# Performance work log

Hardware: AMD Instinct MI355X
Metric: run time of the kernel (lower is better)

Reference implementation:

```python
import jax, jax.numpy as jnp
import numpy as np

D_MODEL = 1024
NUM_HEADS = 16
D_HEAD = 64
D_MLP = 4096
SEQ = 2048
BATCH = 4
NEG_BIG = 1e10


def setup_inputs() -> dict:
    key = jax.random.key(0)
    ks = jax.random.split(key, 10)
    s = 1.0 / np.sqrt(D_MODEL)
    return {
        "x": jax.random.normal(ks[0], (BATCH, SEQ, D_MODEL), dtype=jnp.float32),
        "W_K": jax.random.normal(ks[1], (NUM_HEADS, D_HEAD, D_MODEL), dtype=jnp.float32) * s,
        "W_Q": jax.random.normal(ks[2], (NUM_HEADS, D_HEAD, D_MODEL), dtype=jnp.float32) * s,
        "W_V": jax.random.normal(ks[3], (NUM_HEADS, D_HEAD, D_MODEL), dtype=jnp.float32) * s,
        "W_O": jax.random.normal(ks[4], (D_MODEL, D_HEAD * NUM_HEADS), dtype=jnp.float32) * s,
        "W_in": jax.random.normal(ks[5], (D_MLP, D_MODEL), dtype=jnp.float32) * s,
        "b_in": jnp.zeros((D_MLP,), dtype=jnp.float32),
        "W_out": jax.random.normal(ks[6], (D_MODEL, D_MLP), dtype=jnp.float32) * s,
        "b_out": jnp.zeros((D_MODEL,), dtype=jnp.float32),
    }


def _block(x, W_K, W_Q, W_V, W_O, W_in, b_in, W_out, b_out):
    seq = x.shape[1]
    # Attention
    k = jnp.einsum("ihd,bpd->biph", W_K, x)
    q = jnp.einsum("ihd,bpd->biph", W_Q, x)
    v = jnp.einsum("ihd,bpd->biph", W_V, x)
    scores = jnp.einsum("biph,biqh->biqp", k, q)  # [b, i, q(query), p(key)]
    mask = jnp.tril(jnp.ones((seq, seq), dtype=x.dtype))  # causal: key p <= query q
    scores = scores * mask - NEG_BIG * (1.0 - mask)
    attn = jax.nn.softmax(scores / np.sqrt(D_HEAD), axis=-1)
    z = jnp.einsum("biph,biqp->biqh", v, attn)  # [b, heads, q, d_head]
    z_flat = jnp.transpose(z, (0, 2, 1, 3)).reshape(z.shape[0], seq, -1)  # b q (i h)
    attn_out = jnp.einsum("df,bqf->bqd", W_O, z_flat)
    x = x + attn_out
    # MLP
    h = jnp.einsum("md,bpd->bpm", W_in, x) + b_in
    h = jax.nn.gelu(h, approximate=False)
    mlp_out = jnp.einsum("dm,bpm->bpd", W_out, h) + b_out
    return x + mlp_out


def reference(x, W_K, W_Q, W_V, W_O, W_in, b_in, W_out, b_out):
    return _block(x, W_K, W_Q, W_V, W_O, W_in, b_in, W_out, b_out)
```

## Files before the change

kernel.cpp:

```cpp
#include <hip/hip_runtime.h>
#include <hip/hip_bf16.h>

typedef __bf16 bf16;
typedef __bf16 bf16x8 __attribute__((ext_vector_type(8)));
typedef __bf16 bf16x4 __attribute__((ext_vector_type(4)));
typedef float  f32x4  __attribute__((ext_vector_type(4)));

#define MFMA(a,b,c) __builtin_amdgcn_mfma_f32_16x16x32_bf16(a,b,c,0,0,0)
#define EXP2F(x) __builtin_amdgcn_exp2f(x)

__device__ __forceinline__ void gload16(const void* g, void* l) {
  __builtin_amdgcn_global_load_lds((__attribute__((address_space(1))) void*)(g),
                                   (__attribute__((address_space(3))) void*)(l), 16, 0, 0);
}

struct CastSegs {
  const float* src[7];
  bf16* dst[7];
  int cum[8];
};

__global__ void cast_multi(CastSegs s) {
  int i = blockIdx.x * 256 + threadIdx.x;
  if (i >= s.cum[7]) return;
  int k = 0;
  #pragma unroll
  for (int j = 1; j < 7; ++j) if (i >= s.cum[j]) k = j;
  int off = i - s.cum[k];
  const float4* p = (const float4*)s.src[k];
  float4 a = p[2*off], b = p[2*off+1];
  bf16x8 v;
  v[0]=(bf16)a.x; v[1]=(bf16)a.y; v[2]=(bf16)a.z; v[3]=(bf16)a.w;
  v[4]=(bf16)b.x; v[5]=(bf16)b.y; v[6]=(bf16)b.z; v[7]=(bf16)b.w;
  *(bf16x8*)(s.dst[k] + (size_t)8*off) = v;
}

__device__ __forceinline__ float gelu_t(float s) {
  float u = s * (0.7978845608f + 0.0356774081f * s * s);
  return s / (1.0f + EXP2F(-2.885390082f * u));
}

#define LGKM0_FENCE() { asm volatile("s_waitcnt lgkmcnt(0)" ::: "memory"); \
                        __builtin_amdgcn_sched_barrier(0); }


#define LDA_PH(MI2) { _Pragma("unroll") for (int i = 0; i < 4; i++) { \
    af[i][0] = *(const bf16x8*)(lds + ab + ((((MI2)<<2)+i) << 11) + rdswz); \
    af[i][1] = *(const bf16x8*)(lds + ab + ((((MI2)<<2)+i) << 11) + 1024 + rdswz); } }

#define LDB_PH(NI2) { _Pragma("unroll") for (int n = 0; n < 2; n++) { \
    bfr[((NI2)<<1)+n][0] = *(const bf16x8*)(lds + bb + (((((NI2)<<1)+n)) << 11) + rdswz); \
    bfr[((NI2)<<1)+n][1] = *(const bf16x8*)(lds + bb + (((((NI2)<<1)+n)) << 11) + 1024 + rdswz); } }

#define MM_PH(MI2, NI2) { __builtin_amdgcn_s_setprio(1); \
    _Pragma("unroll") for (int i = 0; i < 4; i++) \
      _Pragma("unroll") for (int n = 0; n < 2; n++) { \
        acc[((MI2)<<2)+i][((NI2)<<1)+n] = MFMA(af[i][0], bfr[((NI2)<<1)+n][0], acc[((MI2)<<2)+i][((NI2)<<1)+n]); \
        acc[((MI2)<<2)+i][((NI2)<<1)+n] = MFMA(af[i][1], bfr[((NI2)<<1)+n][1], acc[((MI2)<<2)+i][((NI2)<<1)+n]); } \
    __builtin_amdgcn_s_setprio(0); }

#define GTILE(CUR, S1, S2, VM) { \
    const int ab = ((CUR) << 16) + (wm << 14); \
    const int bb = ((CUR) << 16) + 32768 + (wn << 13); \
    LDA_PH(0); LDB_PH(0); \
    if (S1) STG(sA, (CUR)^1, 0, 1, t + 1); \
    asm volatile("s_waitcnt lgkmcnt(8)" ::: "memory"); \
    __builtin_amdgcn_s_barrier(); LGKM0_FENCE(); \
    MM_PH(0, 0); \
    LDB_PH(1); \
    if (S2) STG(sB, (CUR), 1, 0, t + 2); \
    __builtin_amdgcn_s_barrier(); LGKM0_FENCE(); \
    MM_PH(0, 1); \
    LDA_PH(1); \
    if (S2) STG(sB, (CUR), 1, 1, t + 2); \
    __builtin_amdgcn_s_barrier(); LGKM0_FENCE(); \
    MM_PH(1, 0); \
    if (S2) STG(sA, (CUR), 0, 0, t + 2); \
    MM_PH(1, 1); \
    asm volatile("s_waitcnt vmcnt(" #VM ")" ::: "memory"); \
    __builtin_amdgcn_s_barrier(); \
    __builtin_amdgcn_sched_barrier(0); }

template<int EPI>
__global__ __launch_bounds__(512, 2) void gemm256(
    const bf16* __restrict__ A, const bf16* __restrict__ B,
    float* __restrict__ outf, bf16* __restrict__ outb,
    const bf16* __restrict__ addb, const float* __restrict__ bias,
    bf16* __restrict__ vtb,
    int M, int N, int K, int gx)
{
  __shared__ __attribute__((aligned(128))) char lds[131072];
  const int tid = threadIdx.x;
  const int w = tid >> 6, l = tid & 63, lg = l >> 4, li = l & 15;
  const int wm = w >> 2, wn = w & 3;

  const int nwg = gridDim.x, orig = blockIdx.x;
  const int q = nwg >> 3, r = nwg & 7;
  const int xcd = orig & 7, pos = orig >> 3;
  const int wg = (xcd < r ? xcd*(q+1) : r*(q+1) + (xcd-r)*q) + pos;
  const int m0 = (wg / gx) << 8, n0 = (wg % gx) << 8;

  const int NT = K >> 6;

  const int srow = ((tid >> 7) << 4) + ((tid >> 2) & 15);
  const int scol = (((tid >> 6) & 1) << 5) + (((tid & 3) << 3) ^ (((tid >> 5) & 1) << 4));
  const bf16* sA = A + (size_t)(m0 + srow) * K + scol;
  const bf16* sB = B + (size_t)(n0 + srow) * K + scol;
  char* const myl = lds + (w << 10);

  auto STG = [&](const bf16* s0, int buf, int isB, int h, int tt) {
    const bf16* g = s0 + ((size_t)(h << 7)) * K + ((size_t)tt << 6);
    char* lb = myl + (buf << 16) + (isB << 15) + (h << 14);
    gload16(g, lb);
    gload16(g + ((size_t)K << 6), lb + 8192);
  };

  const int rdswz = (li << 6) + ((lg << 4) ^ ((li & 8) << 2));

  f32x4 acc[8][4] = {};
  bf16x8 af[4][2], bfr[4][2];

  STG(sB, 0, 1, 0, 0); STG(sB, 0, 1, 1, 0); STG(sA, 0, 0, 0, 0); STG(sA, 0, 0, 1, 0);
  asm volatile("s_waitcnt vmcnt(4)" ::: "memory");
  STG(sB, 1, 1, 0, 1); STG(sB, 1, 1, 1, 1); STG(sA, 1, 0, 0, 1);
  asm volatile("s_waitcnt vmcnt(6)" ::: "memory");
  __builtin_amdgcn_s_barrier();
  __builtin_amdgcn_sched_barrier(0);

  int t = 0;
  for (int tt = 0; tt + 3 < NT; tt += 2) {
    t = tt;     GTILE(0, 1, 1, 6);
    t = tt + 1; GTILE(1, 1, 1, 6);
  }
  t = NT - 2; GTILE(0, 1, 0, 0);
  t = NT - 1; GTILE(1, 0, 0, 0);

  if (EPI == 0 && n0 >= 2048) {
    #pragma unroll
    for (int mi = 0; mi < 8; mi++) {
      const int row = m0 + (wm << 7) + (mi << 4) + (lg << 2);
      const int p = row & 2047;
      const size_t bhb = (size_t)((row >> 11) << 4);
      #pragma unroll
      for (int ni = 0; ni < 4; ni++) {
        const int col = n0 + (wn << 6) + (ni << 4) + li;
        const int hh = (col >> 6) & 15, dd = col & 63;
        bf16x4 pk;
        pk[0] = (bf16)acc[mi][ni][0]; pk[1] = (bf16)acc[mi][ni][1];
        pk[2] = (bf16)acc[mi][ni][2]; pk[3] = (bf16)acc[mi][ni][3];
        *(bf16x4*)(vtb + ((bhb + hh) * 64 + dd) * 2048 + p) = pk;
      }
    }
    return;
  }

  #pragma unroll
  for (int mi = 0; mi < 8; mi++) {
    const int row = m0 + (wm << 7) + (mi << 4) + (lg << 2);
    #pragma unroll
    for (int ni = 0; ni < 4; ni++) {
      const int col = n0 + (wn << 6) + (ni << 4) + li;
      #pragma unroll
      for (int r2 = 0; r2 < 4; r2++) {
        const size_t idx = (size_t)(row + r2) * N + col;
        float v = acc[mi][ni][r2];
        if (EPI == 0) {
          outb[idx] = (bf16)v;
        } else if (EPI == 1) {
          outb[idx] = (bf16)(v + (float)addb[idx]);
        } else if (EPI == 2) {
          outb[idx] = (bf16)gelu_t(v + bias[col]);
        } else {
          outf[idx] = v + bias[col] + (float)addb[idx];
        }
      }
    }
  }
}

#define N_LDA2(BMI) { _Pragma("unroll") for (int i = 0; i < 2; i++) { \
    af[i][0] = *(const bf16x8*)(lds + abase + (((BMI)+i) << 11) + rdswz); \
    af[i][1] = *(const bf16x8*)(lds + abase + (((BMI)+i) << 11) + 1024 + rdswz); } }

#define N_LDB2(BNI) { _Pragma("unroll") for (int n = 0; n < 2; n++) { \
    bfr[(BNI)+n][0] = *(const bf16x8*)(lds + bbase + (((BNI)+n) << 11) + rdswz); \
    bfr[(BNI)+n][1] = *(const bf16x8*)(lds + bbase + (((BNI)+n) << 11) + 1024 + rdswz); } }

#define N_MMQ(MB, NB) { __builtin_amdgcn_s_setprio(1); \
    _Pragma("unroll") for (int i = 0; i < 2; i++) \
      _Pragma("unroll") for (int n = 0; n < 2; n++) { \
        acc[((MB)<<1)+i][((NB)<<1)+n] = MFMA(af[i][0], bfr[((NB)<<1)+n][0], acc[((MB)<<1)+i][((NB)<<1)+n]); \
        acc[((MB)<<1)+i][((NB)<<1)+n] = MFMA(af[i][1], bfr[((NB)<<1)+n][1], acc[((MB)<<1)+i][((NB)<<1)+n]); } \
    __builtin_amdgcn_s_setprio(0); }

#define NTILE(CUR, S1, S2, VM) { \
    const int abase = (CUR) * 49152 + ((wm >> 1) << 14) + ((wm & 1) << 13); \
    const int bbase = (CUR) * 49152 + 32768 + (wn << 13); \
    N_LDA2(0); N_LDB2(0); \
    if (S1) STA((CUR)^1, 1, t + 1); \
    __builtin_amdgcn_s_barrier(); LGKM0_FENCE(); \
    N_MMQ(0, 0); \
    N_LDB2(2); \
    if (S2) STB((CUR), 0, t + 2); \
    __builtin_amdgcn_s_barrier(); LGKM0_FENCE(); \
    N_MMQ(0, 1); \
    N_LDA2(2); \
    if (S2) STB((CUR), 1, t + 2); \
    __builtin_amdgcn_s_barrier(); LGKM0_FENCE(); \
    N_MMQ(1, 0); \
    if (S2) STA((CUR), 0, t + 2); \
    N_MMQ(1, 1); \
    asm volatile("s_waitcnt vmcnt(" #VM ")" ::: "memory"); \
    __builtin_amdgcn_s_barrier(); \
    __builtin_amdgcn_sched_barrier(0); }

template<int EPI>
__global__ __launch_bounds__(512, 2) void gemm128n(
    const bf16* __restrict__ A, const bf16* __restrict__ B,
    float* __restrict__ outf, bf16* __restrict__ outb,
    const bf16* __restrict__ addb, const float* __restrict__ bias,
    bf16* __restrict__ vtb,
    int M, int N, int K, int gx)
{
  __shared__ __attribute__((aligned(128))) char lds[98304];
  const int tid = threadIdx.x;
  const int w = tid >> 6, l = tid & 63, lg = l >> 4, li = l & 15;
  const int wm = w >> 1, wn = w & 1;

  const int nwg = gridDim.x, orig = blockIdx.x;
  const int q = nwg >> 3, r = nwg & 7;
  const int xcd = orig & 7, pos = orig >> 3;
  const int wg = (xcd < r ? xcd*(q+1) : r*(q+1) + (xcd-r)*q) + pos;
  const int m0 = (wg / gx) << 8, n0 = (wg % gx) << 7;

  const int NT = K >> 6;

  const int srow = ((tid >> 7) << 4) + ((tid >> 2) & 15);
  const int scol = (((tid >> 6) & 1) << 5) + (((tid & 3) << 3) ^ (((tid >> 5) & 1) << 4));
  const bf16* sA = A + (size_t)(m0 + srow) * K + scol;
  const bf16* sB = B + (size_t)(n0 + srow) * K + scol;
  char* const myl = lds + (w << 10);

  auto STA = [&](int buf, int h, int tt) {
    const bf16* g = sA + ((size_t)(h << 7)) * K + ((size_t)tt << 6);
    char* lb = myl + buf * 49152 + (h << 14);
    gload16(g, lb);
    gload16(g + ((size_t)K << 6), lb + 8192);
  };
  auto STB = [&](int buf, int h, int tt) {
    const bf16* g = sB + ((size_t)(h << 6)) * K + ((size_t)tt << 6);
    gload16(g, myl + buf * 49152 + 32768 + (h << 13));
  };

  const int rdswz = (li << 6) + ((lg << 4) ^ ((li & 8) << 2));

  f32x4 acc[4][4] = {};
  bf16x8 af[2][2], bfr[4][2];

  STB(0, 0, 0); STB(0, 1, 0); STA(0, 0, 0); STA(0, 1, 0);
  STB(1, 0, 1); STB(1, 1, 1); STA(1, 0, 1);
  asm volatile("s_waitcnt vmcnt(4)" ::: "memory");
  __builtin_amdgcn_s_barrier();
  __builtin_amdgcn_sched_barrier(0);

  int t = 0;
  for (int tt = 0; tt + 3 < NT; tt += 2) {
    t = tt;     NTILE(0, 1, 1, 4);
    t = tt + 1; NTILE(1, 1, 1, 4);
  }
  t = NT - 2; NTILE(0, 1, 0, 0);
  t = NT - 1; NTILE(1, 0, 0, 0);

  if (EPI == 0 && n0 >= 2048) {
    #pragma unroll
    for (int mi = 0; mi < 4; mi++) {
      const int row = m0 + (wm << 6) + (mi << 4) + (lg << 2);
      const int p = row & 2047;
      const size_t bhb = (size_t)((row >> 11) << 4);
      #pragma unroll
      for (int ni = 0; ni < 4; ni++) {
        const int col = n0 + (wn << 6) + (ni << 4) + li;
        const int hh = (col >> 6) & 15, dd = col & 63;
        bf16x4 pk;
        pk[0] = (bf16)acc[mi][ni][0]; pk[1] = (bf16)acc[mi][ni][1];
        pk[2] = (bf16)acc[mi][ni][2]; pk[3] = (bf16)acc[mi][ni][3];
        *(bf16x4*)(vtb + ((bhb + hh) * 64 + dd) * 2048 + p) = pk;
      }
    }
    return;
  }

  #pragma unroll
  for (int mi = 0; mi < 4; mi++) {
    const int row = m0 + (wm << 6) + (mi << 4) + (lg << 2);
    #pragma unroll
    for (int ni = 0; ni < 4; ni++) {
      const int col = n0 + (wn << 6) + (ni << 4) + li;
      #pragma unroll
      for (int r2 = 0; r2 < 4; r2++) {
        const size_t idx = (size_t)(row + r2) * N + col;
        float v = acc[mi][ni][r2];
        if (EPI == 0) {
          outb[idx] = (bf16)v;
        } else if (EPI == 1) {
          outb[idx] = (bf16)(v + (float)addb[idx]);
        } else if (EPI == 2) {
          outb[idx] = (bf16)gelu_t(v + bias[col]);
        } else {
          outf[idx] = v + bias[col] + (float)addb[idx];
        }
      }
    }
  }
}

__global__ __launch_bounds__(256) void attn_kernel(const bf16* __restrict__ qkv,
                                                   const bf16* __restrict__ vt,
                                                   bf16* __restrict__ z)
{
  __shared__ bf16 Ksh[2][64*64];
  __shared__ bf16 Vsh[2][64*64];
  __shared__ bf16 Pl[4*16*64];

  const int tid = threadIdx.x;
  const int w = tid >> 6, l = tid & 63, lg = l >> 4, li = l & 15;
  const int orig = blockIdx.x;
  const int xcd = orig & 7, sub = orig >> 3;
  const int bh = (xcd << 3) + (sub >> 4);
  const int pr = sub & 15;
  const int h = bh & 15, b = bh >> 4;
  const size_t tb = (size_t)b * 2048;

  const int srow = tid >> 3, sc = tid & 7;
  const bf16* Kg = qkv + (tb + srow) * 3072 + 1024 + (h << 6) + ((sc ^ (srow & 7)) << 3);
  const bf16* Vg = vt + ((size_t)bh * 64 + srow) * 2048 + ((sc ^ (srow & 7)) << 3);

  char* pw = (char*)Pl + (w << 11) + li * 128;
  const int psw = (li & 3) << 5;

  for (int hf = 0; hf < 2; ++hf) {
    const int qt = hf ? pr : (31 - pr);
    const int qw = (qt << 6) + (w << 4);

    const bf16* Qp = qkv + (tb + qw + li) * 3072 + (h << 6);
    bf16x8 qa0 = *(const bf16x8*)(Qp + (lg << 3));
    bf16x8 qa1 = *(const bf16x8*)(Qp + 32 + (lg << 3));
    #pragma unroll
    for (int e = 0; e < 8; e++) {
      qa0[e] = (bf16)((float)qa0[e] * 0.1803368801f);
      qa1[e] = (bf16)((float)qa1[e] * 0.1803368801f);
    }

    f32x4 zacc[4] = {};
    float lS = 0.f;
    const int nkt = qt + 1;

    gload16(Kg,                   (bf16*)Ksh[0] + (w << 9));
    gload16(Kg + (size_t)32*3072, (bf16*)Ksh[0] + 2048 + (w << 9));
    gload16(Vg,                   (bf16*)Vsh[0] + (w << 9));
    gload16(Vg + (size_t)32*2048, (bf16*)Vsh[0] + 2048 + (w << 9));
    __syncthreads();

    for (int kt = 0; kt < nkt; ++kt) {
      const int cur = kt & 1;
      const int pb = kt << 6;

      if (kt + 1 < nkt) {
        const int nb = cur ^ 1;
        const size_t ko = (size_t)(pb + 64) * 3072;
        gload16(Kg + ko,                   (bf16*)Ksh[nb] + (w << 9));
        gload16(Kg + ko + (size_t)32*3072, (bf16*)Ksh[nb] + 2048 + (w << 9));
        gload16(Vg + pb + 64,                   (bf16*)Vsh[nb] + (w << 9));
        gload16(Vg + pb + 64 + (size_t)32*2048, (bf16*)Vsh[nb] + 2048 + (w << 9));
      }

      f32x4 s[4];
      __builtin_amdgcn_s_setprio(1);
      #pragma unroll
      for (int sub2 = 0; sub2 < 4; ++sub2) {
        const char* kr = (const char*)Ksh[cur] + ((sub2 << 4) + li) * 128;
        const int c0 = (lg ^ (li & 7)) << 4;
        bf16x8 kb0 = *(const bf16x8*)(kr + c0);
        bf16x8 kb1 = *(const bf16x8*)(kr + (c0 ^ 64));
        f32x4 a2 = {};
        a2 = MFMA(kb0, qa0, a2);
        a2 = MFMA(kb1, qa1, a2);
        s[sub2] = a2;
      }
      __builtin_amdgcn_s_setprio(0);

      if (pb + 63 > qw) {
        #pragma unroll
        for (int sub2 = 0; sub2 < 4; ++sub2)
          #pragma unroll
          for (int r = 0; r < 4; ++r)
            if (pb + (sub2 << 4) + (lg << 2) + r > qw + li) s[sub2][r] = -1e30f;
      }

      f32x4 p[4];
      #pragma unroll
      for (int sub2 = 0; sub2 < 4; ++sub2)
        #pragma unroll
        for (int r = 0; r < 4; ++r)
          p[sub2][r] = EXP2F(s[sub2][r]);
      f32x4 t4 = p[0] + p[1] + p[2] + p[3];
      lS += (t4[0] + t4[1]) + (t4[2] + t4[3]);

      #pragma unroll
      for (int sub2 = 0; sub2 < 4; ++sub2) {
        bf16x4 pk;
        pk[0] = (bf16)p[sub2][0]; pk[1] = (bf16)p[sub2][1];
        pk[2] = (bf16)p[sub2][2]; pk[3] = (bf16)p[sub2][3];
        *(bf16x4*)(pw + (((sub2 << 5) + (lg << 3)) ^ psw)) = pk;
      }

      __builtin_amdgcn_s_setprio(1);
      #pragma unroll
      for (int kc = 0; kc < 2; ++kc) {
        bf16x8 pa = *(const bf16x8*)(pw + (((kc << 6) + (lg << 4)) ^ psw));
        #pragma unroll
        for (int d = 0; d < 4; ++d) {
          const char* vr = (const char*)Vsh[cur] + ((d << 4) + li) * 128;
          bf16x8 vb = *(const bf16x8*)(vr + ((((kc << 2) + lg) ^ (li & 7)) << 4));
          zacc[d] = MFMA(pa, vb, zacc[d]);
        }
      }
      __builtin_amdgcn_s_setprio(0);

      __syncthreads();
    }

    lS += __shfl_xor(lS, 16);
    lS += __shfl_xor(lS, 32);

    float rls[4];
    #pragma unroll
    for (int r = 0; r < 4; ++r) rls[r] = 1.0f / __shfl(lS, (lg << 2) + r);
    bf16* zp = z + (tb + qw) * 1024 + (h << 6);
    #pragma unroll
    for (int d = 0; d < 4; ++d)
      #pragma unroll
      for (int r = 0; r < 4; ++r)
        zp[(size_t)((lg << 2) + r) * 1024 + (d << 4) + li] = (bf16)(zacc[d][r] * rls[r]);
  }
}

extern "C" void kernel_launch(void* const* d_in, const int* in_sizes, int n_in,
                              void* d_out, int out_size, void* d_ws, size_t ws_size,
                              hipStream_t stream)
{
  const float* x     = (const float*)d_in[0];
  const float* W_K   = (const float*)d_in[1];
  const float* W_Q   = (const float*)d_in[2];
  const float* W_V   = (const float*)d_in[3];
  const float* W_O   = (const float*)d_in[4];
  const float* W_in  = (const float*)d_in[5];
  const float* b_in  = (const float*)d_in[6];
  const float* W_out = (const float*)d_in[7];
  const float* b_out = (const float*)d_in[8];
  float* out = (float*)d_out;

  char* ws = (char*)d_ws;
  bf16*  xb   = (bf16*)ws;  ws += (size_t)8192*1024*2;
  bf16*  wqkv = (bf16*)ws;  ws += (size_t)3072*1024*2;
  bf16*  wo   = (bf16*)ws;  ws += (size_t)1024*1024*2;
  bf16*  win  = (bf16*)ws;  ws += (size_t)4096*1024*2;
  bf16*  wout = (bf16*)ws;  ws += (size_t)1024*4096*2;
  bf16*  qkv  = (bf16*)ws;  ws += (size_t)8192*3072*2;
  bf16*  zb   = (bf16*)ws;  ws += (size_t)8192*1024*2;
  bf16*  x1b  = (bf16*)ws;  ws += (size_t)8192*1024*2;
  bf16*  hb   = (bf16*)ws;
  bf16*  vtb  = hb;

  CastSegs cs;
  const float* srcs[7] = { x, W_Q, W_K, W_V, W_O, W_in, W_out };
  bf16* dsts[7] = { xb, wqkv, wqkv + 1024*1024, wqkv + 2048*1024, wo, win, wout };
  int n8s[7] = { 1048576, 131072, 131072, 131072, 131072, 524288, 524288 };
  int cum = 0;
  for (int i = 0; i < 7; ++i) { cs.src[i] = srcs[i]; cs.dst[i] = dsts[i]; cs.cum[i] = cum; cum += n8s[i]; }
  cs.cum[7] = cum;
  cast_multi<<<dim3((cum + 255) / 256), dim3(256), 0, stream>>>(cs);

  gemm128n<0><<<dim3(768), 512, 0, stream>>>(xb, wqkv, nullptr, qkv, nullptr, nullptr, vtb, 8192, 3072, 1024, 24);
  attn_kernel<<<dim3(1024), 256, 0, stream>>>(qkv, vtb, zb);
  gemm128n<1><<<dim3(256), 512, 0, stream>>>(zb, wo, nullptr, x1b, xb, nullptr, nullptr, 8192, 1024, 1024, 8);
  gemm256<2><<<dim3(512), 512, 0, stream>>>(x1b, win, nullptr, hb, nullptr, b_in, nullptr, 8192, 4096, 1024, 16);
  gemm128n<3><<<dim3(256), 512, 0, stream>>>(hb, wout, out, nullptr, x1b, b_out, nullptr, 8192, 1024, 4096, 8);
}
```

Measured before the change: 290.6 us.

## Double attention query tile per block to reuse K/V LDS tiles

Each attention block now handles 128 query rows instead of 64, with each wave processing two 16-row groups. Every K/V tile loaded into LDS therefore feeds twice as many MFMAs, which halves global K/V traffic and the number of barriers per query. The grid shrinks from 1024 to 512 blocks, and the P staging buffer in LDS doubles. In exchange, per-wave register pressure rises and there are fewer blocks to balance the causal workload across CUs.

New measurement: 325.9 us. 12.1% more time.

```diff
diff --git a/kernel.cpp b/kernel.cpp
--- a/kernel.cpp
+++ b/kernel.cpp
@@ -320,14 +320,14 @@
 {
   __shared__ bf16 Ksh[2][64*64];
   __shared__ bf16 Vsh[2][64*64];
-  __shared__ bf16 Pl[4*16*64];
+  __shared__ bf16 Pl[4*32*64];
 
   const int tid = threadIdx.x;
   const int w = tid >> 6, l = tid & 63, lg = l >> 4, li = l & 15;
   const int orig = blockIdx.x;
   const int xcd = orig & 7, sub = orig >> 3;
-  const int bh = (xcd << 3) + (sub >> 4);
-  const int pr = sub & 15;
+  const int bh = (xcd << 3) + (sub >> 3);
+  const int pr = sub & 7;
   const int h = bh & 15, b = bh >> 4;
   const size_t tb = (size_t)b * 2048;
 
@@ -335,25 +335,29 @@
   const bf16* Kg = qkv + (tb + srow) * 3072 + 1024 + (h << 6) + ((sc ^ (srow & 7)) << 3);
   const bf16* Vg = vt + ((size_t)bh * 64 + srow) * 2048 + ((sc ^ (srow & 7)) << 3);
 
-  char* pw = (char*)Pl + (w << 11) + li * 128;
+  char* pw = (char*)Pl + (w << 12) + li * 128;
   const int psw = (li & 3) << 5;
 
   for (int hf = 0; hf < 2; ++hf) {
-    const int qt = hf ? pr : (31 - pr);
-    const int qw = (qt << 6) + (w << 4);
-
-    const bf16* Qp = qkv + (tb + qw + li) * 3072 + (h << 6);
-    bf16x8 qa0 = *(const bf16x8*)(Qp + (lg << 3));
-    bf16x8 qa1 = *(const bf16x8*)(Qp + 32 + (lg << 3));
+    const int qt = hf ? pr : (15 - pr);
+    const int qw = (qt << 7) + (w << 5);
+
+    bf16x8 qa0[2], qa1[2];
     #pragma unroll
-    for (int e = 0; e < 8; e++) {
-      qa0[e] = (bf16)((float)qa0[e] * 0.1803368801f);
-      qa1[e] = (bf16)((float)qa1[e] * 0.1803368801f);
-    }
-
-    f32x4 zacc[4] = {};
-    float lS = 0.f;
-    const int nkt = qt + 1;
+    for (int g = 0; g < 2; ++g) {
+      const bf16* Qp = qkv + (tb + qw + (g << 4) + li) * 3072 + (h << 6);
+      qa0[g] = *(const bf16x8*)(Qp + (lg << 3));
+      qa1[g] = *(const bf16x8*)(Qp + 32 + (lg << 3));
+      #pragma unroll
+      for (int e = 0; e < 8; e++) {
+        qa0[g][e] = (bf16)((float)qa0[g][e] * 0.1803368801f);
+        qa1[g][e] = (bf16)((float)qa1[g][e] * 0.1803368801f);
+      }
+    }
+
+    f32x4 zacc[2][4] = {};
+    float lS0 = 0.f, lS1 = 0.f;
+    const int nkt = (qt + 1) << 1;
 
     gload16(Kg,                   (bf16*)Ksh[0] + (w << 9));
     gload16(Kg + (size_t)32*3072, (bf16*)Ksh[0] + 2048 + (w << 9));
@@ -374,7 +378,7 @@
         gload16(Vg + pb + 64 + (size_t)32*2048, (bf16*)Vsh[nb] + 2048 + (w << 9));
       }
 
-      f32x4 s[4];
+      f32x4 s[2][4];
       __builtin_amdgcn_s_setprio(1);
       #pragma unroll
       for (int sub2 = 0; sub2 < 4; ++sub2) {
@@ -382,47 +386,58 @@
         const int c0 = (lg ^ (li & 7)) << 4;
         bf16x8 kb0 = *(const bf16x8*)(kr + c0);
         bf16x8 kb1 = *(const bf16x8*)(kr + (c0 ^ 64));
-        f32x4 a2 = {};
-        a2 = MFMA(kb0, qa0, a2);
-        a2 = MFMA(kb1, qa1, a2);
-        s[sub2] = a2;
+        #pragma unroll
+        for (int g = 0; g < 2; ++g) {
+          f32x4 a2 = {};
+          a2 = MFMA(kb0, qa0[g], a2);
+          a2 = MFMA(kb1, qa1[g], a2);
+          s[g][sub2] = a2;
+        }
       }
       __builtin_amdgcn_s_setprio(0);
 
       if (pb + 63 > qw) {
+        #pragma unroll
+        for (int g = 0; g < 2; ++g)
+          #pragma unroll
+          for (int sub2 = 0; sub2 < 4; ++sub2)
+            #pragma unroll
+            for (int r = 0; r < 4; ++r)
+              if (pb + (sub2 << 4) + (lg << 2) + r > qw + (g << 4) + li)
+                s[g][sub2][r] = -1e30f;
+      }
+
+      #pragma unroll
+      for (int g = 0; g < 2; ++g) {
+        f32x4 p[4];
         #pragma unroll
         for (int sub2 = 0; sub2 < 4; ++sub2)
           #pragma unroll
           for (int r = 0; r < 4; ++r)
-            if (pb + (sub2 << 4) + (lg << 2) + r > qw + li) s[sub2][r] = -1e30f;
-      }
-
-      f32x4 p[4];
-      #pragma unroll
-      for (int sub2 = 0; sub2 < 4; ++sub2)
+            p[sub2][r] = EXP2F(s[g][sub2][r]);
+        f32x4 t4 = p[0] + p[1] + p[2] + p[3];
+        float sm = (t4[0] + t4[1]) + (t4[2] + t4[3]);
+        if (g == 0) lS0 += sm; else lS1 += sm;
         #pragma unroll
-        for (int r = 0; r < 4; ++r)
-          p[sub2][r] = EXP2F(s[sub2][r]);
-      f32x4 t4 = p[0] + p[1] + p[2] + p[3];
-      lS += (t4[0] + t4[1]) + (t4[2] + t4[3]);
-
-      #pragma unroll
-      for (int sub2 = 0; sub2 < 4; ++sub2) {
-        bf16x4 pk;
-        pk[0] = (bf16)p[sub2][0]; pk[1] = (bf16)p[sub2][1];
-        pk[2] = (bf16)p[sub2][2]; pk[3] = (bf16)p[sub2][3];
-        *(bf16x4*)(pw + (((sub2 << 5) + (lg << 3)) ^ psw)) = pk;
+        for (int sub2 = 0; sub2 < 4; ++sub2) {
+          bf16x4 pk;
+          pk[0] = (bf16)p[sub2][0]; pk[1] = (bf16)p[sub2][1];
+          pk[2] = (bf16)p[sub2][2]; pk[3] = (bf16)p[sub2][3];
+          *(bf16x4*)(pw + (g << 11) + (((sub2 << 5) + (lg << 3)) ^ psw)) = pk;
+        }
       }
 
       __builtin_amdgcn_s_setprio(1);
       #pragma unroll
       for (int kc = 0; kc < 2; ++kc) {
-        bf16x8 pa = *(const bf16x8*)(pw + (((kc << 6) + (lg << 4)) ^ psw));
+        bf16x8 pa0 = *(const bf16x8*)(pw + (((kc << 6) + (lg << 4)) ^ psw));
+        bf16x8 pa1 = *(const bf16x8*)(pw + 2048 + (((kc << 6) + (lg << 4)) ^ psw));
         #pragma unroll
         for (int d = 0; d < 4; ++d) {
           const char* vr = (const char*)Vsh[cur] + ((d << 4) + li) * 128;
           bf16x8 vb = *(const bf16x8*)(vr + ((((kc << 2) + lg) ^ (li & 7)) << 4));
-          zacc[d] = MFMA(pa, vb, zacc[d]);
+          zacc[0][d] = MFMA(pa0, vb, zacc[0][d]);
+          zacc[1][d] = MFMA(pa1, vb, zacc[1][d]);
         }
       }
       __builtin_amdgcn_s_setprio(0);
@@ -430,18 +445,24 @@
       __syncthreads();
     }
 
-    lS += __shfl_xor(lS, 16);
-    lS += __shfl_xor(lS, 32);
-
-    float rls[4];
+    lS0 += __shfl_xor(lS0, 16);
+    lS0 += __shfl_xor(lS0, 32);
+    lS1 += __shfl_xor(lS1, 16);
+    lS1 += __shfl_xor(lS1, 32);
+
     #pragma unroll
-    for (int r = 0; r < 4; ++r) rls[r] = 1.0f / __shfl(lS, (lg << 2) + r);
-    bf16* zp = z + (tb + qw) * 1024 + (h << 6);
-    #pragma unroll
-    for (int d = 0; d < 4; ++d)
+    for (int g = 0; g < 2; ++g) {
+      float rls[4];
       #pragma unroll
       for (int r = 0; r < 4; ++r)
-        zp[(size_t)((lg << 2) + r) * 1024 + (d << 4) + li] = (bf16)(zacc[d][r] * rls[r]);
+        rls[r] = 1.0f / __shfl(g == 0 ? lS0 : lS1, (lg << 2) + r);
+      bf16* zp = z + (tb + qw + (g << 4)) * 1024 + (h << 6);
+      #pragma unroll
+      for (int d = 0; d < 4; ++d)
+        #pragma unroll
+        for (int r = 0; r < 4; ++r)
+          zp[(size_t)((lg << 2) + r) * 1024 + (d << 4) + li] = (bf16)(zacc[g][d][r] * rls[r]);
+    }
   }
 }
 
@@ -482,7 +503,7 @@
   cast_multi<<<dim3((cum + 255) / 256), dim3(256), 0, stream>>>(cs);
 
   gemm128n<0><<<dim3(768), 512, 0, stream>>>(xb, wqkv, nullptr, qkv, nullptr, nullptr, vtb, 8192, 3072, 1024, 24);
-  attn_kernel<<<dim3(1024), 256, 0, stream>>>(qkv, vtb, zb);
+  attn_kernel<<<dim3(512), 256, 0, stream>>>(qkv, vtb, zb);
   gemm128n<1><<<dim3(256), 512, 0, stream>>>(zb, wo, nullptr, x1b, xb, nullptr, nullptr, 8192, 1024, 1024, 8);
   gemm256<2><<<dim3(512), 512, 0, stream>>>(x1b, win, nullptr, hb, nullptr, b_in, nullptr, 8192, 4096, 1024, 16);
   gemm128n<3><<<dim3(256), 512, 0, stream>>>(hb, wout, out, nullptr, x1b, b_out, nullptr, 8192, 1024, 4096, 8);
```

## Add 128x128 square-tile GEMM for output projection and MLP-out GEMMs

Applied to the files above, without the earlier changes.

Adds a new gemm128sq kernel that uses 128x128 output tiles with 8 waves laid out 4x2, each wave computing 32x64. It uses double-buffered direct-to-LDS loads and software pipelining across two tiles per loop iteration. The W_O and W_out GEMMs (N=1024) now launch 512 workgroups instead of 256, which gives more parallelism on a machine with many CUs. The cost is less reuse per tile, since each workgroup computes fewer outputs per byte loaded, and more barriers per K step.

Result: slower. 297.6 us (+2.4%).

```diff
diff --git a/kernel.cpp b/kernel.cpp
--- a/kernel.cpp
+++ b/kernel.cpp
@@ -308,6 +308,117 @@
           outb[idx] = (bf16)gelu_t(v + bias[col]);
         } else {
           outf[idx] = v + bias[col] + (float)addb[idx];
+        }
+      }
+    }
+  }
+}
+
+#define S_LDA(MI) { _Pragma("unroll") for (int kc = 0; kc < 2; kc++) \
+    af[MI][kc] = *(const bf16x8*)(lds + abase + ((((wm & 1) << 1) + (MI)) << 11) + kc * 1024 + rdswz); }
+
+#define S_LDB(NI2) { _Pragma("unroll") for (int n = 0; n < 2; n++) \
+    _Pragma("unroll") for (int kc = 0; kc < 2; kc++) \
+    bfr[((NI2)<<1)+n][kc] = *(const bf16x8*)(lds + bbase + ((((NI2)<<1)+n) << 11) + kc * 1024 + rdswz); }
+
+#define S_MMQ(MB, NB) { __builtin_amdgcn_s_setprio(1); \
+    _Pragma("unroll") for (int n = 0; n < 2; n++) { \
+      acc[MB][((NB)<<1)+n] = MFMA(af[MB][0], bfr[((NB)<<1)+n][0], acc[MB][((NB)<<1)+n]); \
+      acc[MB][((NB)<<1)+n] = MFMA(af[MB][1], bfr[((NB)<<1)+n][1], acc[MB][((NB)<<1)+n]); } \
+    __builtin_amdgcn_s_setprio(0); }
+
+#define SQTILE(CUR, S1, S2, VM) { \
+    const int abase = ((CUR) << 15) + ((wm >> 1) << 13); \
+    const int bbase = ((CUR) << 15) + 16384 + (wn << 13); \
+    S_LDA(0); S_LDB(0); \
+    if (S1) STA((CUR)^1, 1, t + 1); \
+    __builtin_amdgcn_s_barrier(); LGKM0_FENCE(); \
+    S_MMQ(0, 0); \
+    S_LDB(1); \
+    __builtin_amdgcn_s_barrier(); LGKM0_FENCE(); \
+    S_MMQ(0, 1); \
+    S_LDA(1); \
+    if (S2) STB((CUR), 0, t + 2); \
+    __builtin_amdgcn_s_barrier(); LGKM0_FENCE(); \
+    S_MMQ(1, 0); \
+    if (S2) { STB((CUR), 1, t + 2); STA((CUR), 0, t + 2); } \
+    S_MMQ(1, 1); \
+    asm volatile("s_waitcnt vmcnt(" #VM ")" ::: "memory"); \
+    __builtin_amdgcn_s_barrier(); \
+    __builtin_amdgcn_sched_barrier(0); }
+
+template<int EPI>
+__global__ __launch_bounds__(512, 4) void gemm128sq(
+    const bf16* __restrict__ A, const bf16* __restrict__ B,
+    float* __restrict__ outf, bf16* __restrict__ outb,
+    const bf16* __restrict__ addb, const float* __restrict__ bias,
+    int M, int N, int K, int gx)
+{
+  __shared__ __attribute__((aligned(128))) char lds[65536];
+  const int tid = threadIdx.x;
+  const int w = tid >> 6, l = tid & 63, lg = l >> 4, li = l & 15;
+  const int wm = w >> 1, wn = w & 1;
+
+  const int nwg = gridDim.x, orig = blockIdx.x;
+  const int q = nwg >> 3, r = nwg & 7;
+  const int xcd = orig & 7, pos = orig >> 3;
+  const int wg = (xcd < r ? xcd*(q+1) : r*(q+1) + (xcd-r)*q) + pos;
+  const int m0 = (wg / gx) << 7, n0 = (wg % gx) << 7;
+
+  const int NT = K >> 6;
+
+  const int srow = ((tid >> 7) << 4) + ((tid >> 2) & 15);
+  const int scol = (((tid >> 6) & 1) << 5) + (((tid & 3) << 3) ^ (((tid >> 5) & 1) << 4));
+  const bf16* sA = A + (size_t)(m0 + srow) * K + scol;
+  const bf16* sB = B + (size_t)(n0 + srow) * K + scol;
+  char* const myl = lds + (w << 10);
+
+  auto STA = [&](int buf, int h, int tt) {
+    gload16(sA + ((size_t)(h << 6)) * K + ((size_t)tt << 6),
+            myl + (buf << 15) + (h << 13));
+  };
+  auto STB = [&](int buf, int h, int tt) {
+    gload16(sB + ((size_t)(h << 6)) * K + ((size_t)tt << 6),
+            myl + (buf << 15) + 16384 + (h << 13));
+  };
+
+  const int rdswz = (li << 6) + ((lg << 4) ^ ((li & 8) << 2));
+
+  f32x4 acc[2][4] = {};
+  bf16x8 af[2][2], bfr[4][2];
+
+  STB(0, 0, 0); STB(0, 1, 0); STA(0, 0, 0); STA(0, 1, 0);
+  STB(1, 0, 1); STB(1, 1, 1); STA(1, 0, 1);
+  asm volatile("s_waitcnt vmcnt(3)" ::: "memory");
+  __builtin_amdgcn_s_barrier();
+  __builtin_amdgcn_sched_barrier(0);
+
+  int t = 0;
+  for (int tt = 0; tt + 3 < NT; tt += 2) {
+    t = tt;     SQTILE(0, 1, 1, 3);
+    t = tt + 1; SQTILE(1, 1, 1, 3);
+  }
+  t = NT - 2; SQTILE(0, 1, 0, 0);
+  t = NT - 1; SQTILE(1, 0, 0, 0);
+
+  #pragma unroll
+  for (int mi = 0; mi < 2; mi++) {
+    const int row = m0 + (wm << 5) + (mi << 4) + (lg << 2);
+    #pragma unroll
+    for (int ni = 0; ni < 4; ni++) {
+      const int col = n0 + (wn << 6) + (ni << 4) + li;
+      #pragma unroll
+      for (int r2 = 0; r2 < 4; r2++) {
+        const size_t idx = (size_t)(row + r2) * N + col;
+        float v = acc[mi][ni][r2];
+        if (EPI == 1) {
+          outb[idx] = (bf16)(v + (float)addb[idx]);
+        } else if (EPI == 2) {
+          outb[idx] = (bf16)gelu_t(v + bias[col]);
+        } else if (EPI == 3) {
+          outf[idx] = v + bias[col] + (float)addb[idx];
+        } else {
+          outb[idx] = (bf16)v;
         }
       }
     }
@@ -483,7 +594,7 @@
 
   gemm128n<0><<<dim3(768), 512, 0, stream>>>(xb, wqkv, nullptr, qkv, nullptr, nullptr, vtb, 8192, 3072, 1024, 24);
   attn_kernel<<<dim3(1024), 256, 0, stream>>>(qkv, vtb, zb);
-  gemm128n<1><<<dim3(256), 512, 0, stream>>>(zb, wo, nullptr, x1b, xb, nullptr, nullptr, 8192, 1024, 1024, 8);
+  gemm128sq<1><<<dim3(512), 512, 0, stream>>>(zb, wo, nullptr, x1b, xb, nullptr, 8192, 1024, 1024, 8);
   gemm256<2><<<dim3(512), 512, 0, stream>>>(x1b, win, nullptr, hb, nullptr, b_in, nullptr, 8192, 4096, 1024, 16);
-  gemm128n<3><<<dim3(256), 512, 0, stream>>>(hb, wout, out, nullptr, x1b, b_out, nullptr, 8192, 1024, 4096, 8);
-}
+  gemm128sq<3><<<dim3(512), 512, 0, stream>>>(hb, wout, out, nullptr, x1b, b_out, 8192, 1024, 4096, 8);
+}
```
